# Kernel optimization log

Hardware: AMD Instinct MI355X
Metric: run time of the kernel (lower is better)

Reference implementation:

```python
import jax, jax.numpy as jnp
import numpy as np

B, T, D, H, DH, PD = 4, 1024, 1024, 16, 64, 4
DFF = 4 * D
EPS = 1e-5

# Plucker pair index vectors for point_dim=4: pairs (0,1),(0,2),(0,3),(1,2),(1,3),(2,3)
_PI = jnp.array([0, 0, 0, 1, 1, 2])
_PJ = jnp.array([1, 2, 3, 2, 3, 3])
_J6 = jnp.array([[0,0,0,0,0,1],[0,0,0,0,-1,0],[0,0,0,1,0,0],
                 [0,0,1,0,0,0],[0,-1,0,0,0,0],[1,0,0,0,0,0]], dtype=jnp.float32)

def layer_norm(x, g, b):
    mu = jnp.mean(x, axis=-1, keepdims=True)
    var = jnp.var(x, axis=-1, keepdims=True)
    return (x - mu) * jax.lax.rsqrt(var + EPS) * g + b

def exterior(p1, p2):
    # p1,p2: [B,T,H,4] -> normalized Plucker line [B,T,H,6]
    L = p1[..., _PI] * p2[..., _PJ] - p1[..., _PJ] * p2[..., _PI]
    n = jnp.maximum(jnp.linalg.norm(L, axis=-1, keepdims=True), 1e-12)
    return L / n

def linear(x, w, b=None):
    y = jnp.einsum('...i,oi->...o', x, w)
    return y + b if b is not None else y


def setup_inputs() -> dict:
    key = jax.random.key(0)
    ks = jax.random.split(key, 16)
    s = 0.02
    return {
        'x': jax.random.normal(ks[0], (B, T, D), jnp.float32),
        'ln1_g': jnp.ones((D,), jnp.float32), 'ln1_b': jnp.zeros((D,), jnp.float32),
        'qkv_w': jax.random.normal(ks[1], (3 * D, D), jnp.float32) * s,
        'qkv_b': jnp.zeros((3 * D,), jnp.float32),
        'w1w': jax.random.normal(ks[2], (PD * H, D), jnp.float32) * s,
        'w2w': jax.random.normal(ks[3], (PD * H, D), jnp.float32) * s,
        'w1r': jax.random.normal(ks[4], (PD * H, D), jnp.float32) * s,
        'w2r': jax.random.normal(ks[5], (PD * H, D), jnp.float32) * s,
        'memv_w': jax.random.normal(ks[6], (D, D), jnp.float32) * s,
        'memv_b': jnp.zeros((D,), jnp.float32),
        'memg_w': jax.random.normal(ks[7], (H, D), jnp.float32) * s,
        'memg_b': jnp.zeros((H,), jnp.float32),
        'mem_scale': jnp.full((H,), 0.1, jnp.float32),
        'out_w': jax.random.normal(ks[8], (D, D), jnp.float32) * s,
        'out_b': jnp.zeros((D,), jnp.float32),
        'decay_logits': jnp.full((H,), 4.6, jnp.float32),
        'ln2_g': jnp.ones((D,), jnp.float32), 'ln2_b': jnp.zeros((D,), jnp.float32),
        'fc1_w': jax.random.normal(ks[9], (DFF, D), jnp.float32) * s,
        'fc1_b': jnp.zeros((DFF,), jnp.float32),
        'fc2_w': jax.random.normal(ks[10], (D, DFF), jnp.float32) * s,
        'fc2_b': jnp.zeros((D,), jnp.float32),
    }


def attn_forward(h, qkv_w, qkv_b, w1w, w2w, w1r, w2r, memv_w, memv_b,
                 memg_w, memg_b, mem_scale, out_w, out_b, decay_logits):
    # Standard causal attention (dropout = identity, eval mode)
    qkv = linear(h, qkv_w, qkv_b).reshape(B, T, 3, H, DH)
    q, k, v = [jnp.transpose(qkv[:, :, i], (0, 2, 1, 3)) for i in range(3)]  # [B,H,T,dh]
    scores = jnp.einsum('bhqd,bhkd->bhqk', q, k) * (DH ** -0.5)
    causal_mask = jnp.triu(jnp.ones((T, T), bool), k=1)
    scores = jnp.where(causal_mask, -jnp.inf, scores)
    attn = jax.nn.softmax(scores, axis=-1)
    seq_out = jnp.einsum('bhqk,bhkd->bhqd', attn, v).transpose(0, 2, 1, 3).reshape(B, T, D)

    # Geometric incidence memory branch
    x_prev = jnp.concatenate([jnp.zeros((B, 1, D), h.dtype), h[:, :-1]], axis=1)
    w1 = linear(x_prev, w1w).reshape(B, T, H, PD)
    w2 = linear(h, w2w).reshape(B, T, H, PD)
    write_lines = exterior(w1, w2)                   # [B,T,H,6]
    r1 = linear(h, w1r).reshape(B, T, H, PD)
    r2 = linear(h, w2r).reshape(B, T, H, PD)
    read_lines = exterior(r1, r2)                    # [B,T,H,6]
    J_write = jnp.einsum('bthi,ij->bthj', write_lines, _J6)
    incidence = jnp.einsum('bihp,bjhp->bhij', read_lines, J_write)  # [B,H,T,T]
    inc_abs = jnp.abs(incidence)

    # per-head exponential decay over strictly-past positions (i > j)
    decays = jax.nn.sigmoid(decay_logits)            # [H]
    pos = jnp.arange(T, dtype=h.dtype)
    diffs = pos[:, None] - pos[None, :]              # [T,T]
    past = diffs > 0
    # decays**diffs, masked to strictly-past (subsumes the causal masked_fill on inc_abs)
    weights = jnp.where(past, decays[:, None, None] ** jnp.maximum(diffs, 0.0), 0.0)  # [H,T,T]
    mem_score = jnp.einsum('bhij,hij->bhi', inc_abs, weights)  # [B,H,T]

    mem_val = linear(h, memv_w, memv_b)              # [B,T,D]
    gate = jax.nn.sigmoid(linear(h, memg_w, memg_b)) # [B,T,H]
    gated = jax.nn.sigmoid(mem_score.transpose(0, 2, 1) * mem_scale) * gate
    gated = jnp.mean(gated, axis=-1, keepdims=True)  # [B,T,1]
    return linear(seq_out + gated * mem_val, out_w, out_b)


def reference(x, ln1_g, ln1_b, qkv_w, qkv_b, w1w, w2w, w1r, w2r,
              memv_w, memv_b, memg_w, memg_b, mem_scale, out_w, out_b,
              decay_logits, ln2_g, ln2_b, fc1_w, fc1_b, fc2_w, fc2_b):
    # Pre-LN transformer block: x + Attn(LN(x)); x + MLP(LN(x))
    h = layer_norm(x, ln1_g, ln1_b)
    x = x + attn_forward(h, qkv_w, qkv_b, w1w, w2w, w1r, w2r, memv_w, memv_b,
                         memg_w, memg_b, mem_scale, out_w, out_b, decay_logits)
    h2 = layer_norm(x, ln2_g, ln2_b)
    mlp = linear(jax.nn.gelu(linear(h2, fc1_w, fc1_b), approximate=False), fc2_w, fc2_b)
    return x + mlp
```

## Files before the change

kernel.cpp:

```cpp
#include <hip/hip_runtime.h>
#include <math.h>

typedef __bf16 bf16;
typedef float f32x4 __attribute__((ext_vector_type(4)));
typedef bf16 bf16x8 __attribute__((ext_vector_type(8)));
typedef bf16 bf16x4 __attribute__((ext_vector_type(4)));

#define DEV __device__ __forceinline__

DEV void async16(const void* g, void* s) {
  __builtin_amdgcn_global_load_lds(
      (const __attribute__((address_space(1))) unsigned int*)g,
      (__attribute__((address_space(3))) unsigned int*)s, 16, 0, 0);
}

DEV f32x4 mfma16(bf16x8 a, bf16x8 b, f32x4 c) {
  return __builtin_amdgcn_mfma_f32_16x16x32_bf16(a, b, c, 0, 0, 0);
}

DEV float sigf(float x) { return 1.0f / (1.0f + __expf(-x)); }

__global__ __launch_bounds__(256)
void cast_w_k(const float* __restrict__ qkv_w, const float* __restrict__ w1w,
              const float* __restrict__ w2w, const float* __restrict__ w1r,
              const float* __restrict__ w2r, const float* __restrict__ memg_w,
              const float* __restrict__ memv_w, const float* __restrict__ out_w,
              const float* __restrict__ fc1_w, const float* __restrict__ fc2_w,
              bf16* __restrict__ dst)
{
  const long i = ((long)blockIdx.x * 256 + threadIdx.x) * 4;
  if (i >= 14024704L) return;
  float4 v;
  if      (i < 3145728L)  v = *(const float4*)&qkv_w[i];
  else if (i < 3211264L)  v = *(const float4*)&w1w[i - 3145728L];
  else if (i < 3276800L)  v = *(const float4*)&w2w[i - 3211264L];
  else if (i < 3342336L)  v = *(const float4*)&w1r[i - 3276800L];
  else if (i < 3407872L)  v = *(const float4*)&w2r[i - 3342336L];
  else if (i < 3424256L)  v = *(const float4*)&memg_w[i - 3407872L];
  else if (i < 3538944L)  v = make_float4(0.f, 0.f, 0.f, 0.f);
  else if (i < 4587520L)  v = *(const float4*)&memv_w[i - 3538944L];
  else if (i < 5636096L)  v = *(const float4*)&out_w[i - 4587520L];
  else if (i < 9830400L)  v = *(const float4*)&fc1_w[i - 5636096L];
  else                    v = *(const float4*)&fc2_w[i - 9830400L];
  bf16x4 y;
  y[0] = (bf16)v.x; y[1] = (bf16)v.y; y[2] = (bf16)v.z; y[3] = (bf16)v.w;
  *(bf16x4*)&dst[i] = y;
}

__global__ __launch_bounds__(256)
void ln_k(const float* __restrict__ x, const float* __restrict__ g,
          const float* __restrict__ bb, bf16* __restrict__ out)
{
  const int row = blockIdx.x, tid = threadIdx.x;
  const float4 xv = ((const float4*)(x + (long)row * 1024))[tid];
  float s  = xv.x + xv.y + xv.z + xv.w;
  float ss = xv.x * xv.x + xv.y * xv.y + xv.z * xv.z + xv.w * xv.w;
#pragma unroll
  for (int off = 1; off < 64; off <<= 1) {
    s  += __shfl_xor(s, off);
    ss += __shfl_xor(ss, off);
  }
  __shared__ float red[8];
  const int wave = tid >> 6, lane = tid & 63;
  if (lane == 0) { red[wave] = s; red[4 + wave] = ss; }
  __syncthreads();
  s  = red[0] + red[1] + red[2] + red[3];
  ss = red[4] + red[5] + red[6] + red[7];
  const float mu  = s * (1.0f / 1024.0f);
  const float var = ss * (1.0f / 1024.0f) - mu * mu;
  const float inv = rsqrtf(var + 1e-5f);
  const float4 gv = ((const float4*)g)[tid];
  const float4 bv = ((const float4*)bb)[tid];
  bf16x4 y;
  y[0] = (bf16)((xv.x - mu) * inv * gv.x + bv.x);
  y[1] = (bf16)((xv.y - mu) * inv * gv.y + bv.y);
  y[2] = (bf16)((xv.z - mu) * inv * gv.z + bv.z);
  y[3] = (bf16)((xv.w - mu) * inv * gv.w + bv.w);
  *(bf16x4*)&out[(long)row * 1024 + tid * 4] = y;
}

enum { M_BIAS_RES = 0, M_GELU = 1 };

#define GEMM_CORE(Aptr, Bptr, Kloop, Kstride)                                \
  __shared__ __align__(16) bf16 As[128 * 32];                                \
  __shared__ __align__(16) bf16 Bs[128 * 32];                                \
  const int tid = threadIdx.x;                                               \
  const int wave = tid >> 6, lane = tid & 63;                                \
  const int fr = lane & 15, fq = lane >> 4;                                  \
  const long bm = (long)blockIdx.y * 128;                                    \
  const long bn = (long)blockIdx.x * 128;                                    \
  const int wm = (wave >> 1) * 64, wn = (wave & 1) * 64;                     \
  const int sr = wave * 16 + (lane >> 2);                                    \
  const int sc = (lane & 3) * 8;                                             \
  const bf16* ag0 = Aptr + (bm + sr) * (long)Kstride + sc;                   \
  const bf16* ag1 = Aptr + (bm + 64 + sr) * (long)Kstride + sc;              \
  const bf16* bg0 = Bptr + (bn + sr) * (long)Kstride + sc;                   \
  const bf16* bg1 = Bptr + (bn + 64 + sr) * (long)Kstride + sc;              \
  bf16* as0 = &As[(wave * 16) * 32];                                         \
  bf16* as1 = &As[(64 + wave * 16) * 32];                                    \
  bf16* bs0 = &Bs[(wave * 16) * 32];                                         \
  bf16* bs1 = &Bs[(64 + wave * 16) * 32];                                    \
  f32x4 acc[4][4] = {};                                                      \
  for (int kt = 0; kt < Kloop; kt += 32) {                                   \
    __syncthreads();                                                         \
    async16(ag0 + kt, as0);                                                  \
    async16(ag1 + kt, as1);                                                  \
    async16(bg0 + kt, bs0);                                                  \
    async16(bg1 + kt, bs1);                                                  \
    __syncthreads();                                                         \
    bf16x8 af[4], bfr[4];                                                    \
    _Pragma("unroll")                                                        \
    for (int i = 0; i < 4; ++i)                                              \
      af[i] = *(const bf16x8*)&As[(wm + i * 16 + fr) * 32 + fq * 8];         \
    _Pragma("unroll")                                                        \
    for (int j = 0; j < 4; ++j)                                              \
      bfr[j] = *(const bf16x8*)&Bs[(wn + j * 16 + fr) * 32 + fq * 8];        \
    _Pragma("unroll")                                                        \
    for (int i = 0; i < 4; ++i)                                              \
      _Pragma("unroll")                                                      \
      for (int j = 0; j < 4; ++j)                                            \
        acc[i][j] = mfma16(af[i], bfr[j], acc[i][j]);                        \
  }

template <int MODE>
__global__ __launch_bounds__(256, 2)
void gemm_k(const bf16* __restrict__ A, const bf16* __restrict__ Bw,
            int N, int K,
            const float* __restrict__ bias, const float* __restrict__ res,
            float* __restrict__ outf, bf16* __restrict__ outb)
{
  GEMM_CORE(A, Bw, K, K)
#pragma unroll
  for (int i = 0; i < 4; ++i) {
    const long row0 = bm + wm + i * 16 + fq * 4;
#pragma unroll
    for (int j = 0; j < 4; ++j) {
      const long col = bn + wn + j * 16 + fr;
#pragma unroll
      for (int r = 0; r < 4; ++r) {
        const long rr = row0 + r;
        float v = acc[i][j][r];
        if (MODE == M_BIAS_RES) {
          outf[rr * N + col] = v + bias[col] + res[rr * N + col];
        } else {
          v += bias[col];
          v = 0.5f * v * (1.0f + erff(v * 0.70710678118654752f));
          outb[rr * N + col] = (bf16)v;
        }
      }
    }
  }
}

__global__ __launch_bounds__(256, 2)
void gemm_fc2_k(const bf16* __restrict__ A_, const bf16* __restrict__ Bw_,
                float* __restrict__ part)
{
  const bf16* A  = A_  + (long)blockIdx.z * 2048;
  const bf16* Bw = Bw_ + (long)blockIdx.z * 2048;
  float* outf = part + (long)blockIdx.z * 4194304;
  GEMM_CORE(A, Bw, 2048, 4096)
#pragma unroll
  for (int i = 0; i < 4; ++i) {
    const long row0 = bm + wm + i * 16 + fq * 4;
#pragma unroll
    for (int j = 0; j < 4; ++j) {
      const long col = bn + wn + j * 16 + fr;
#pragma unroll
      for (int r = 0; r < 4; ++r)
        outf[(row0 + r) * 1024 + col] = acc[i][j][r];
    }
  }
}

__global__ __launch_bounds__(256)
void fc2red_k(const float* __restrict__ part, const float* __restrict__ x2,
              const float* __restrict__ fc2_b, float* __restrict__ out)
{
  const long row = blockIdx.x;
  const int tid = threadIdx.x;
  const long idx = row * 1024 + tid * 4;
  const float4 p0 = *(const float4*)&part[idx];
  const float4 p1 = *(const float4*)&part[idx + 4194304];
  const float4 xv = *(const float4*)&x2[idx];
  const float4 bv = *(const float4*)&fc2_b[tid * 4];
  float4 o;
  o.x = p0.x + p1.x + xv.x + bv.x;
  o.y = p0.y + p1.y + xv.y + bv.y;
  o.z = p0.z + p1.z + xv.z + bv.z;
  o.w = p0.w + p1.w + xv.w + bv.w;
  *(float4*)&out[idx] = o;
}

__global__ __launch_bounds__(256, 2)
void gemm3_k(const bf16* __restrict__ A, const bf16* __restrict__ Bw,
             const float* __restrict__ qkv_b, const float* __restrict__ memv_b,
             bf16* __restrict__ qk_out ,
             bf16* __restrict__ vt_out ,
             float* __restrict__ w4out ,
             float* __restrict__ memval )
{
  GEMM_CORE(A, Bw, 1024, 1024)
  if (bn < 3072) {
#pragma unroll
    for (int i = 0; i < 4; ++i) {
      const long row0 = bm + wm + i * 16 + fq * 4;
      const long b = row0 >> 10, t0 = row0 & 1023;
#pragma unroll
      for (int j = 0; j < 4; ++j) {
        const long col = bn + wn + j * 16 + fr;
        const long i3 = col >> 10;
        const long hh = (col >> 6) & 15;
        const long d  = col & 63;
        const float bs = qkv_b[col];
        if (i3 == 2) {
          bf16x4 y;
#pragma unroll
          for (int r = 0; r < 4; ++r) y[r] = (bf16)(acc[i][j][r] + bs);
          *(bf16x4*)&vt_out[((b * 16 + hh) * 64 + d) * 1024 + t0] = y;
        } else {
          const float sc2 = (i3 == 0) ? 0.125f : 1.0f;
          const long base = i3 * 4194304 + ((b * 16 + hh) * 1024 + t0) * 64 + d;
#pragma unroll
          for (int r = 0; r < 4; ++r)
            qk_out[base + r * 64] = (bf16)((acc[i][j][r] + bs) * sc2);
        }
      }
    }
  } else if (bn < 3456) {
#pragma unroll
    for (int i = 0; i < 4; ++i) {
      const long row0 = bm + wm + i * 16 + fq * 4;
#pragma unroll
      for (int j = 0; j < 4; ++j) {
        const long col = bn + wn + j * 16 + fr - 3072;
#pragma unroll
        for (int r = 0; r < 4; ++r)
          w4out[(row0 + r) * 384 + col] = acc[i][j][r];
      }
    }
  } else {
#pragma unroll
    for (int i = 0; i < 4; ++i) {
      const long row0 = bm + wm + i * 16 + fq * 4;
#pragma unroll
      for (int j = 0; j < 4; ++j) {
        const long col = bn + wn + j * 16 + fr - 3456;
        const float bs = memv_b[col];
#pragma unroll
        for (int r = 0; r < 4; ++r)
          memval[(row0 + r) * 1024 + col] = acc[i][j][r] + bs;
      }
    }
  }
}

__global__ __launch_bounds__(256, 3)
void attn_k(const bf16* __restrict__ q, const bf16* __restrict__ k,
            const bf16* __restrict__ vt, float* __restrict__ seq)
{
  __shared__ __align__(16) bf16 Ks[64 * 72];
  __shared__ __align__(16) bf16 Vs[64 * 72];
  __shared__ __align__(16) bf16 Ps[4][16 * 72];
  const int bx = blockIdx.x, h = blockIdx.y, b = blockIdx.z;
  const int tid = threadIdx.x;
  const int wave = tid >> 6, lane = tid & 63;
  const int fr = lane & 15, fq = lane >> 4;
  const long bh  = ((long)b * 16 + h) * 1024;
  const long bhv = ((long)b * 16 + h) * 64;

  for (int pass = 0; pass < 2; ++pass) {
    const int qt = pass ? 15 - bx : bx;
    const int qbase = qt * 64;
    const bf16x8 aq0 = *(const bf16x8*)&q[(bh + qbase + wave * 16 + fr) * 64 + fq * 8];
    const bf16x8 aq1 = *(const bf16x8*)&q[(bh + qbase + wave * 16 + fr) * 64 + 32 + fq * 8];

    f32x4 o[4] = {};
    float m_r[4] = {-1e30f, -1e30f, -1e30f, -1e30f};
    float l_r[4] = {0.0f, 0.0f, 0.0f, 0.0f};

    for (int kt = 0; kt <= qt; ++kt) {
      const int kb = kt * 64;
      __syncthreads();
#pragma unroll
      for (int rep = 0; rep < 2; ++rep) {
        const int c = rep * 256 + tid;
        const int key = c >> 3, seg = c & 7;
        *(bf16x8*)&Ks[key * 72 + seg * 8] =
            *(const bf16x8*)&k[(bh + kb + key) * 64 + seg * 8];
      }
#pragma unroll
      for (int rep = 0; rep < 2; ++rep) {
        const int c = rep * 256 + tid;
        const int d = c >> 3, seg = c & 7;
        *(bf16x8*)&Vs[d * 72 + seg * 8] =
            *(const bf16x8*)&vt[(bhv + d) * 1024 + kb + seg * 8];
      }
      __syncthreads();

      f32x4 s[4];
#pragma unroll
      for (int j = 0; j < 4; ++j) {
        const bf16x8 b0 = *(const bf16x8*)&Ks[(j * 16 + fr) * 72 + fq * 8];
        const bf16x8 b1 = *(const bf16x8*)&Ks[(j * 16 + fr) * 72 + 32 + fq * 8];
        f32x4 tacc = {};
        tacc = mfma16(aq0, b0, tacc);
        tacc = mfma16(aq1, b1, tacc);
        s[j] = tacc;
      }
      if (kt == qt) {
#pragma unroll
        for (int j = 0; j < 4; ++j)
#pragma unroll
          for (int r = 0; r < 4; ++r)
            if (kb + j * 16 + fr > qbase + wave * 16 + fq * 4 + r) s[j][r] = -1e30f;
      }

      float alpha[4];
#pragma unroll
      for (int r = 0; r < 4; ++r) {
        float t = fmaxf(fmaxf(s[0][r], s[1][r]), fmaxf(s[2][r], s[3][r]));
#pragma unroll
        for (int off = 1; off < 16; off <<= 1) t = fmaxf(t, __shfl_xor(t, off));
        const float mn = fmaxf(m_r[r], t);
        alpha[r] = __expf(m_r[r] - mn);
        m_r[r] = mn;
        float ls = 0.0f;
#pragma unroll
        for (int j = 0; j < 4; ++j) {
          const float p = __expf(s[j][r] - mn);
          s[j][r] = p;
          ls += p;
        }
#pragma unroll
        for (int off = 1; off < 16; off <<= 1) ls += __shfl_xor(ls, off);
        l_r[r] = l_r[r] * alpha[r] + ls;
#pragma unroll
        for (int jd = 0; jd < 4; ++jd) o[jd][r] *= alpha[r];
      }

#pragma unroll
      for (int j = 0; j < 4; ++j)
#pragma unroll
        for (int r = 0; r < 4; ++r)
          Ps[wave][(fq * 4 + r) * 72 + j * 16 + fr] = (bf16)s[j][r];

      const bf16x8 ap0 = *(const bf16x8*)&Ps[wave][fr * 72 + fq * 8];
      const bf16x8 ap1 = *(const bf16x8*)&Ps[wave][fr * 72 + 32 + fq * 8];
#pragma unroll
      for (int jd = 0; jd < 4; ++jd) {
        const bf16x8 b0 = *(const bf16x8*)&Vs[(jd * 16 + fr) * 72 + fq * 8];
        const bf16x8 b1 = *(const bf16x8*)&Vs[(jd * 16 + fr) * 72 + 32 + fq * 8];
        o[jd] = mfma16(ap0, b0, o[jd]);
        o[jd] = mfma16(ap1, b1, o[jd]);
      }
    }

#pragma unroll
    for (int r = 0; r < 4; ++r) {
      const long t_ = qbase + wave * 16 + fq * 4 + r;
      const float inv = 1.0f / l_r[r];
#pragma unroll
      for (int jd = 0; jd < 4; ++jd)
        seq[((long)b * 1024 + t_) * 1024 + h * 64 + jd * 16 + fr] = o[jd][r] * inv;
    }
  }
}

DEV void ext6(const float* p1, const float* p2, float* out) {
  const float L0 = p1[0] * p2[1] - p1[1] * p2[0];
  const float L1 = p1[0] * p2[2] - p1[2] * p2[0];
  const float L2 = p1[0] * p2[3] - p1[3] * p2[0];
  const float L3 = p1[1] * p2[2] - p1[2] * p2[1];
  const float L4 = p1[1] * p2[3] - p1[3] * p2[1];
  const float L5 = p1[2] * p2[3] - p1[3] * p2[2];
  const float nrm = sqrtf(L0*L0 + L1*L1 + L2*L2 + L3*L3 + L4*L4 + L5*L5);
  const float inv = 1.0f / fmaxf(nrm, 1e-12f);
  out[0] = L0 * inv; out[1] = L1 * inv; out[2] = L2 * inv;
  out[3] = L3 * inv; out[4] = L4 * inv; out[5] = L5 * inv;
}

__global__ __launch_bounds__(256)
void lines_k(const float* __restrict__ w4o, float* __restrict__ rl,
             float* __restrict__ jw)
{
  const int idx = blockIdx.x * 256 + threadIdx.x;
  const int hh = idx & 15;
  const int n  = idx >> 4;
  const int t  = n & 1023;
  const int b  = n >> 10;
  float p1[4], p2[4], wl[6], rv[6];
  if (t == 0) { p1[0] = p1[1] = p1[2] = p1[3] = 0.0f; }
  else {
    const float* s = w4o + (long)(n - 1) * 384 + hh * 4;
    p1[0] = s[0]; p1[1] = s[1]; p1[2] = s[2]; p1[3] = s[3];
  }
  { const float* s = w4o + (long)n * 384 + 64 + hh * 4;
    p2[0] = s[0]; p2[1] = s[1]; p2[2] = s[2]; p2[3] = s[3]; }
  ext6(p1, p2, wl);
  { const float* s = w4o + (long)n * 384 + 128 + hh * 4;
    p1[0] = s[0]; p1[1] = s[1]; p1[2] = s[2]; p1[3] = s[3]; }
  { const float* s = w4o + (long)n * 384 + 192 + hh * 4;
    p2[0] = s[0]; p2[1] = s[1]; p2[2] = s[2]; p2[3] = s[3]; }
  ext6(p1, p2, rv);
  const long dst = (((long)b * 16 + hh) * 1024 + t) * 6;
  jw[dst + 0] =  wl[5]; jw[dst + 1] = -wl[4]; jw[dst + 2] =  wl[3];
  jw[dst + 3] =  wl[2]; jw[dst + 4] = -wl[1]; jw[dst + 5] =  wl[0];
  rl[dst + 0] = rv[0]; rl[dst + 1] = rv[1]; rl[dst + 2] = rv[2];
  rl[dst + 3] = rv[3]; rl[dst + 4] = rv[4]; rl[dst + 5] = rv[5];
}

__global__ __launch_bounds__(256)
void memscore_k(const float* __restrict__ rl, const float* __restrict__ jw,
                const float* __restrict__ decay_logits, float* __restrict__ ms)
{
  __shared__ __align__(16) float jwS[256 * 8];
  const int IT[10] = {0,1,1,2,2,2,3,3,3,3};
  const int JC[10] = {0,0,1,0,1,2,0,1,2,3};
  const int it = IT[blockIdx.x], jc = JC[blockIdx.x];
  const int bh = blockIdx.y, hh = bh & 15;
  const float d = sigf(decay_logits[hh]);
  const float invd = 1.0f / d;
  const int j0 = jc * 256;
  const float* jwp = jw + (long)bh * 6144 + (long)j0 * 6;
#pragma unroll
  for (int rep = 0; rep < 8; ++rep) {
    const int c = rep * 256 + threadIdx.x;
    const int row = c >> 3, col = c & 7;
    jwS[c] = (col < 6) ? jwp[row * 6 + col] : 0.0f;
  }
  __syncthreads();
  const int i = it * 256 + threadIdx.x;
  const float* rlp = rl + (long)bh * 6144 + (long)i * 6;
  const float r0 = rlp[0], r1 = rlp[1], r2 = rlp[2];
  const float r3 = rlp[3], r4 = rlp[4], r5 = rlp[5];
  const int nj = (jc == it) ? (int)threadIdx.x : 256;
  float w = __expf(__logf(d) * (float)(i - j0));
  float s = 0.0f;
  for (int jj = 0; jj < nj; ++jj) {
    const float* row = &jwS[jj * 8];
    const float dot = r0 * row[0] + r1 * row[1] + r2 * row[2] +
                      r3 * row[3] + r4 * row[4] + r5 * row[5];
    s += fabsf(dot) * w;
    w *= invd;
  }
  atomicAdd(&ms[(long)bh * 1024 + i], s);
}

__global__ __launch_bounds__(256)
void combine_k(const float* __restrict__ seq, const float* __restrict__ memval,
               const float* __restrict__ w4o, const float* __restrict__ ms,
               const float* __restrict__ memg_b, const float* __restrict__ mem_scale,
               bf16* __restrict__ comb)
{
  const int n = blockIdx.x;
  const int b = n >> 10, t = n & 1023;
  const int tid = threadIdx.x;
  __shared__ float gsh;
  if (tid < 16) {
    const int hh = tid;
    const float gate = sigf(w4o[(long)n * 384 + 256 + hh] + memg_b[hh]);
    float val = sigf(ms[((long)(b * 16 + hh)) * 1024 + t] * mem_scale[hh]) * gate;
#pragma unroll
    for (int off = 1; off < 16; off <<= 1) val += __shfl_xor(val, off);
    if (tid == 0) gsh = val * (1.0f / 16.0f);
  }
  __syncthreads();
  const float g = gsh;
  const float4 sv = ((const float4*)(seq + (long)n * 1024))[tid];
  const float4 mv = ((const float4*)(memval + (long)n * 1024))[tid];
  bf16x4 y;
  y[0] = (bf16)(sv.x + g * mv.x);
  y[1] = (bf16)(sv.y + g * mv.y);
  y[2] = (bf16)(sv.z + g * mv.z);
  y[3] = (bf16)(sv.w + g * mv.w);
  *(bf16x4*)&comb[(long)n * 1024 + tid * 4] = y;
}

extern "C" void kernel_launch(void* const* d_in, const int* in_sizes, int n_in,
                              void* d_out, int out_size, void* d_ws, size_t ws_size,
                              hipStream_t stream) {
  (void)in_sizes; (void)n_in; (void)out_size; (void)ws_size;
  const float* x         = (const float*)d_in[0];
  const float* ln1_g     = (const float*)d_in[1];
  const float* ln1_b     = (const float*)d_in[2];
  const float* qkv_w     = (const float*)d_in[3];
  const float* qkv_b     = (const float*)d_in[4];
  const float* w1w       = (const float*)d_in[5];
  const float* w2w       = (const float*)d_in[6];
  const float* w1r       = (const float*)d_in[7];
  const float* w2r       = (const float*)d_in[8];
  const float* memv_w    = (const float*)d_in[9];
  const float* memv_b    = (const float*)d_in[10];
  const float* memg_w    = (const float*)d_in[11];
  const float* memg_b    = (const float*)d_in[12];
  const float* mem_scale = (const float*)d_in[13];
  const float* out_w     = (const float*)d_in[14];
  const float* out_b     = (const float*)d_in[15];
  const float* decay_l   = (const float*)d_in[16];
  const float* ln2_g     = (const float*)d_in[17];
  const float* ln2_b     = (const float*)d_in[18];
  const float* fc1_w     = (const float*)d_in[19];
  const float* fc1_b     = (const float*)d_in[20];
  const float* fc2_w     = (const float*)d_in[21];
  const float* fc2_b     = (const float*)d_in[22];

  char* ws = (char*)d_ws;
  bf16*  Wbf    = (bf16*)ws;
  bf16*  Wout   = Wbf + 4587520;
  bf16*  Wfc1   = Wbf + 5636096;
  bf16*  Wfc2   = Wbf + 9830400;
  bf16*  h_bf   = (bf16*)(ws + 28049408);
  bf16*  q_bf   = (bf16*)(ws + 36438016);
  bf16*  vt_bf  = q_bf + 2 * 4194304;
  float* seq    = (float*)(ws + 61603840);
  bf16*  fc1out = q_bf;
  float* w4out  = (float*)(ws + 78381056);
  float* rl     = (float*)(ws + 84672512);
  float* jwb    = (float*)(ws + 86245376);
  float* msb    = (float*)(ws + 87818240);
  float* memval = (float*)(ws + 88080384);
  bf16*  comb   = (bf16*)(ws + 104857600);
  float* x2     = (float*)(ws + 113246208);
  float* fc2part = (float*)(ws + 78381056);

  cast_w_k<<<13696, 256, 0, stream>>>(qkv_w, w1w, w2w, w1r, w2r, memg_w,
                                      memv_w, out_w, fc1_w, fc2_w, Wbf);
  ln_k<<<4096, 256, 0, stream>>>(x, ln1_g, ln1_b, h_bf);
  gemm3_k<<<dim3(35, 32), 256, 0, stream>>>(h_bf, Wbf, qkv_b, memv_b,
                                            q_bf, vt_bf, w4out, memval);
  attn_k<<<dim3(8, 16, 4), 256, 0, stream>>>(q_bf, q_bf + 4194304, vt_bf, seq);
  lines_k<<<256, 256, 0, stream>>>(w4out, rl, jwb);
  hipMemsetAsync(msb, 0, 64 * 1024 * sizeof(float), stream);
  memscore_k<<<dim3(10, 64), 256, 0, stream>>>(rl, jwb, decay_l, msb);
  combine_k<<<4096, 256, 0, stream>>>(seq, memval, w4out, msb, memg_b,
                                      mem_scale, comb);
  gemm_k<M_BIAS_RES><<<dim3(8, 32), 256, 0, stream>>>(comb, Wout, 1024, 1024,
                                                      out_b, x, x2, nullptr);
  ln_k<<<4096, 256, 0, stream>>>(x2, ln2_g, ln2_b, h_bf);
  gemm_k<M_GELU><<<dim3(32, 32), 256, 0, stream>>>(h_bf, Wfc1, 4096, 1024,
                                                   fc1_b, nullptr, nullptr, fc1out);
  gemm_fc2_k<<<dim3(8, 32, 2), 256, 0, stream>>>(fc1out, Wfc2, fc2part);
  fc2red_k<<<4096, 256, 0, stream>>>(fc2part, x2, fc2_b, (float*)d_out);
}
```

Baseline: 440.0 us.

## Fuse memory gating into attention epilogue, split-K out-proj with fused LN2

After: 433.3 us. About the same (-1.5%).

```diff
diff --git a/kernel.cpp b/kernel.cpp
--- a/kernel.cpp
+++ b/kernel.cpp
@@ -77,6 +77,50 @@
   y[2] = (bf16)((xv.z - mu) * inv * gv.z + bv.z);
   y[3] = (bf16)((xv.w - mu) * inv * gv.w + bv.w);
   *(bf16x4*)&out[(long)row * 1024 + tid * 4] = y;
+}
+
+__global__ __launch_bounds__(256)
+void ln2red_k(const float* __restrict__ part, const float* __restrict__ out_b,
+              const float* __restrict__ x, const float* __restrict__ g,
+              const float* __restrict__ bb, float* __restrict__ x2,
+              bf16* __restrict__ h)
+{
+  const int row = blockIdx.x, tid = threadIdx.x;
+  const long idx = (long)row * 1024 + tid * 4;
+  const float4 p0 = *(const float4*)&part[idx];
+  const float4 p1 = *(const float4*)&part[idx + 4194304];
+  const float4 xr = *(const float4*)&x[idx];
+  const float4 ob = *(const float4*)&out_b[tid * 4];
+  float4 xv;
+  xv.x = p0.x + p1.x + xr.x + ob.x;
+  xv.y = p0.y + p1.y + xr.y + ob.y;
+  xv.z = p0.z + p1.z + xr.z + ob.z;
+  xv.w = p0.w + p1.w + xr.w + ob.w;
+  *(float4*)&x2[idx] = xv;
+  float s  = xv.x + xv.y + xv.z + xv.w;
+  float ss = xv.x * xv.x + xv.y * xv.y + xv.z * xv.z + xv.w * xv.w;
+#pragma unroll
+  for (int off = 1; off < 64; off <<= 1) {
+    s  += __shfl_xor(s, off);
+    ss += __shfl_xor(ss, off);
+  }
+  __shared__ float red[8];
+  const int wave = tid >> 6, lane = tid & 63;
+  if (lane == 0) { red[wave] = s; red[4 + wave] = ss; }
+  __syncthreads();
+  s  = red[0] + red[1] + red[2] + red[3];
+  ss = red[4] + red[5] + red[6] + red[7];
+  const float mu  = s * (1.0f / 1024.0f);
+  const float var = ss * (1.0f / 1024.0f) - mu * mu;
+  const float inv = rsqrtf(var + 1e-5f);
+  const float4 gv = ((const float4*)g)[tid];
+  const float4 bv = ((const float4*)bb)[tid];
+  bf16x4 y;
+  y[0] = (bf16)((xv.x - mu) * inv * gv.x + bv.x);
+  y[1] = (bf16)((xv.y - mu) * inv * gv.y + bv.y);
+  y[2] = (bf16)((xv.z - mu) * inv * gv.z + bv.z);
+  y[3] = (bf16)((xv.w - mu) * inv * gv.w + bv.w);
+  *(bf16x4*)&h[idx] = y;
 }
 
 enum { M_BIAS_RES = 0, M_GELU = 1 };
@@ -123,7 +167,7 @@
   }
 
 template <int MODE>
-__global__ __launch_bounds__(256, 2)
+__global__ __launch_bounds__(256, 4)
 void gemm_k(const bf16* __restrict__ A, const bf16* __restrict__ Bw,
             int N, int K,
             const float* __restrict__ bias, const float* __restrict__ res,
@@ -152,14 +196,15 @@
   }
 }
 
-__global__ __launch_bounds__(256, 2)
-void gemm_fc2_k(const bf16* __restrict__ A_, const bf16* __restrict__ Bw_,
-                float* __restrict__ part)
-{
-  const bf16* A  = A_  + (long)blockIdx.z * 2048;
-  const bf16* Bw = Bw_ + (long)blockIdx.z * 2048;
+template <int KLEN, int KSTRIDE>
+__global__ __launch_bounds__(256, 4)
+void gemm_splitk_k(const bf16* __restrict__ A_, const bf16* __restrict__ Bw_,
+                   float* __restrict__ part)
+{
+  const bf16* A  = A_  + (long)blockIdx.z * KLEN;
+  const bf16* Bw = Bw_ + (long)blockIdx.z * KLEN;
   float* outf = part + (long)blockIdx.z * 4194304;
-  GEMM_CORE(A, Bw, 2048, 4096)
+  GEMM_CORE(A, Bw, KLEN, KSTRIDE)
 #pragma unroll
   for (int i = 0; i < 4; ++i) {
     const long row0 = bm + wm + i * 16 + fq * 4;
@@ -192,7 +237,7 @@
   *(float4*)&out[idx] = o;
 }
 
-__global__ __launch_bounds__(256, 2)
+__global__ __launch_bounds__(256, 4)
 void gemm3_k(const bf16* __restrict__ A, const bf16* __restrict__ Bw,
              const float* __restrict__ qkv_b, const float* __restrict__ memv_b,
              bf16* __restrict__ qk_out ,
@@ -257,7 +302,8 @@
 
 __global__ __launch_bounds__(256, 3)
 void attn_k(const bf16* __restrict__ q, const bf16* __restrict__ k,
-            const bf16* __restrict__ vt, float* __restrict__ seq)
+            const bf16* __restrict__ vt, const float* __restrict__ memval,
+            const float* __restrict__ gbuf, bf16* __restrict__ comb)
 {
   __shared__ __align__(16) bf16 Ks[64 * 72];
   __shared__ __align__(16) bf16 Vs[64 * 72];
@@ -359,10 +405,15 @@
 #pragma unroll
     for (int r = 0; r < 4; ++r) {
       const long t_ = qbase + wave * 16 + fq * 4 + r;
+      const long row = (long)b * 1024 + t_;
       const float inv = 1.0f / l_r[r];
-#pragma unroll
-      for (int jd = 0; jd < 4; ++jd)
-        seq[((long)b * 1024 + t_) * 1024 + h * 64 + jd * 16 + fr] = o[jd][r] * inv;
+      const float gv = gbuf[row];
+#pragma unroll
+      for (int jd = 0; jd < 4; ++jd) {
+        const long col = h * 64 + jd * 16 + fr;
+        comb[row * 1024 + col] =
+            (bf16)(o[jd][r] * inv + gv * memval[row * 1024 + col]);
+      }
     }
   }
 }
@@ -381,66 +432,50 @@
 }
 
 __global__ __launch_bounds__(256)
-void lines_k(const float* __restrict__ w4o, float* __restrict__ rl,
-             float* __restrict__ jw)
-{
-  const int idx = blockIdx.x * 256 + threadIdx.x;
-  const int hh = idx & 15;
-  const int n  = idx >> 4;
-  const int t  = n & 1023;
-  const int b  = n >> 10;
-  float p1[4], p2[4], wl[6], rv[6];
-  if (t == 0) { p1[0] = p1[1] = p1[2] = p1[3] = 0.0f; }
-  else {
-    const float* s = w4o + (long)(n - 1) * 384 + hh * 4;
-    p1[0] = s[0]; p1[1] = s[1]; p1[2] = s[2]; p1[3] = s[3];
-  }
-  { const float* s = w4o + (long)n * 384 + 64 + hh * 4;
-    p2[0] = s[0]; p2[1] = s[1]; p2[2] = s[2]; p2[3] = s[3]; }
-  ext6(p1, p2, wl);
-  { const float* s = w4o + (long)n * 384 + 128 + hh * 4;
-    p1[0] = s[0]; p1[1] = s[1]; p1[2] = s[2]; p1[3] = s[3]; }
-  { const float* s = w4o + (long)n * 384 + 192 + hh * 4;
-    p2[0] = s[0]; p2[1] = s[1]; p2[2] = s[2]; p2[3] = s[3]; }
-  ext6(p1, p2, rv);
-  const long dst = (((long)b * 16 + hh) * 1024 + t) * 6;
-  jw[dst + 0] =  wl[5]; jw[dst + 1] = -wl[4]; jw[dst + 2] =  wl[3];
-  jw[dst + 3] =  wl[2]; jw[dst + 4] = -wl[1]; jw[dst + 5] =  wl[0];
-  rl[dst + 0] = rv[0]; rl[dst + 1] = rv[1]; rl[dst + 2] = rv[2];
-  rl[dst + 3] = rv[3]; rl[dst + 4] = rv[4]; rl[dst + 5] = rv[5];
-}
-
-__global__ __launch_bounds__(256)
-void memscore_k(const float* __restrict__ rl, const float* __restrict__ jw,
+void memscore_k(const float* __restrict__ w4o,
                 const float* __restrict__ decay_logits, float* __restrict__ ms)
 {
   __shared__ __align__(16) float jwS[256 * 8];
   const int IT[10] = {0,1,1,2,2,2,3,3,3,3};
   const int JC[10] = {0,0,1,0,1,2,0,1,2,3};
   const int it = IT[blockIdx.x], jc = JC[blockIdx.x];
-  const int bh = blockIdx.y, hh = bh & 15;
+  const int bh = blockIdx.y, hh = bh & 15, b = bh >> 4;
   const float d = sigf(decay_logits[hh]);
   const float invd = 1.0f / d;
   const int j0 = jc * 256;
-  const float* jwp = jw + (long)bh * 6144 + (long)j0 * 6;
-#pragma unroll
-  for (int rep = 0; rep < 8; ++rep) {
-    const int c = rep * 256 + threadIdx.x;
-    const int row = c >> 3, col = c & 7;
-    jwS[c] = (col < 6) ? jwp[row * 6 + col] : 0.0f;
+  {
+    const int j = j0 + threadIdx.x;
+    const long nj = (long)b * 1024 + j;
+    float p1[4], p2[4], wl[6];
+    if (j == 0) { p1[0] = p1[1] = p1[2] = p1[3] = 0.0f; }
+    else {
+      const float* s = w4o + (nj - 1) * 384 + hh * 4;
+      p1[0] = s[0]; p1[1] = s[1]; p1[2] = s[2]; p1[3] = s[3];
+    }
+    { const float* s = w4o + nj * 384 + 64 + hh * 4;
+      p2[0] = s[0]; p2[1] = s[1]; p2[2] = s[2]; p2[3] = s[3]; }
+    ext6(p1, p2, wl);
+    float* dstS = &jwS[threadIdx.x * 8];
+    dstS[0] =  wl[5]; dstS[1] = -wl[4]; dstS[2] =  wl[3];
+    dstS[3] =  wl[2]; dstS[4] = -wl[1]; dstS[5] =  wl[0];
+    dstS[6] = 0.0f;   dstS[7] = 0.0f;
   }
   __syncthreads();
   const int i = it * 256 + threadIdx.x;
-  const float* rlp = rl + (long)bh * 6144 + (long)i * 6;
-  const float r0 = rlp[0], r1 = rlp[1], r2 = rlp[2];
-  const float r3 = rlp[3], r4 = rlp[4], r5 = rlp[5];
+  const long ni = (long)b * 1024 + i;
+  float q1[4], q2[4], rv[6];
+  { const float* s = w4o + ni * 384 + 128 + hh * 4;
+    q1[0] = s[0]; q1[1] = s[1]; q1[2] = s[2]; q1[3] = s[3]; }
+  { const float* s = w4o + ni * 384 + 192 + hh * 4;
+    q2[0] = s[0]; q2[1] = s[1]; q2[2] = s[2]; q2[3] = s[3]; }
+  ext6(q1, q2, rv);
   const int nj = (jc == it) ? (int)threadIdx.x : 256;
   float w = __expf(__logf(d) * (float)(i - j0));
   float s = 0.0f;
   for (int jj = 0; jj < nj; ++jj) {
     const float* row = &jwS[jj * 8];
-    const float dot = r0 * row[0] + r1 * row[1] + r2 * row[2] +
-                      r3 * row[3] + r4 * row[4] + r5 * row[5];
+    const float dot = rv[0] * row[0] + rv[1] * row[1] + rv[2] * row[2] +
+                      rv[3] * row[3] + rv[4] * row[4] + rv[5] * row[5];
     s += fabsf(dot) * w;
     w *= invd;
   }
@@ -448,33 +483,19 @@
 }
 
 __global__ __launch_bounds__(256)
-void combine_k(const float* __restrict__ seq, const float* __restrict__ memval,
-               const float* __restrict__ w4o, const float* __restrict__ ms,
-               const float* __restrict__ memg_b, const float* __restrict__ mem_scale,
-               bf16* __restrict__ comb)
-{
-  const int n = blockIdx.x;
+void gate_k(const float* __restrict__ w4o, const float* __restrict__ ms,
+            const float* __restrict__ memg_b, const float* __restrict__ mem_scale,
+            float* __restrict__ g)
+{
+  const int n = blockIdx.x * 256 + threadIdx.x;
   const int b = n >> 10, t = n & 1023;
-  const int tid = threadIdx.x;
-  __shared__ float gsh;
-  if (tid < 16) {
-    const int hh = tid;
-    const float gate = sigf(w4o[(long)n * 384 + 256 + hh] + memg_b[hh]);
-    float val = sigf(ms[((long)(b * 16 + hh)) * 1024 + t] * mem_scale[hh]) * gate;
-#pragma unroll
-    for (int off = 1; off < 16; off <<= 1) val += __shfl_xor(val, off);
-    if (tid == 0) gsh = val * (1.0f / 16.0f);
-  }
-  __syncthreads();
-  const float g = gsh;
-  const float4 sv = ((const float4*)(seq + (long)n * 1024))[tid];
-  const float4 mv = ((const float4*)(memval + (long)n * 1024))[tid];
-  bf16x4 y;
-  y[0] = (bf16)(sv.x + g * mv.x);
-  y[1] = (bf16)(sv.y + g * mv.y);
-  y[2] = (bf16)(sv.z + g * mv.z);
-  y[3] = (bf16)(sv.w + g * mv.w);
-  *(bf16x4*)&comb[(long)n * 1024 + tid * 4] = y;
+  float acc = 0.0f;
+#pragma unroll
+  for (int h = 0; h < 16; ++h) {
+    const float gate = sigf(w4o[(long)n * 384 + 256 + h] + memg_b[h]);
+    acc += sigf(ms[((long)(b * 16 + h)) * 1024 + t] * mem_scale[h]) * gate;
+  }
+  g[n] = acc * (1.0f / 16.0f);
 }
 
 extern "C" void kernel_launch(void* const* d_in, const int* in_sizes, int n_in,
@@ -513,33 +534,32 @@
   bf16*  h_bf   = (bf16*)(ws + 28049408);
   bf16*  q_bf   = (bf16*)(ws + 36438016);
   bf16*  vt_bf  = q_bf + 2 * 4194304;
-  float* seq    = (float*)(ws + 61603840);
+  float* oppart = (float*)(ws + 36438016);
   bf16*  fc1out = q_bf;
   float* w4out  = (float*)(ws + 78381056);
-  float* rl     = (float*)(ws + 84672512);
-  float* jwb    = (float*)(ws + 86245376);
-  float* msb    = (float*)(ws + 87818240);
+  float* msb    = (float*)(ws + 84672512);
+  float* gbuf   = (float*)(ws + 84934656);
   float* memval = (float*)(ws + 88080384);
+  float* fc2part = (float*)(ws + 69992448);
   bf16*  comb   = (bf16*)(ws + 104857600);
   float* x2     = (float*)(ws + 113246208);
-  float* fc2part = (float*)(ws + 78381056);
 
   cast_w_k<<<13696, 256, 0, stream>>>(qkv_w, w1w, w2w, w1r, w2r, memg_w,
                                       memv_w, out_w, fc1_w, fc2_w, Wbf);
   ln_k<<<4096, 256, 0, stream>>>(x, ln1_g, ln1_b, h_bf);
   gemm3_k<<<dim3(35, 32), 256, 0, stream>>>(h_bf, Wbf, qkv_b, memv_b,
                                             q_bf, vt_bf, w4out, memval);
-  attn_k<<<dim3(8, 16, 4), 256, 0, stream>>>(q_bf, q_bf + 4194304, vt_bf, seq);
-  lines_k<<<256, 256, 0, stream>>>(w4out, rl, jwb);
   hipMemsetAsync(msb, 0, 64 * 1024 * sizeof(float), stream);
-  memscore_k<<<dim3(10, 64), 256, 0, stream>>>(rl, jwb, decay_l, msb);
-  combine_k<<<4096, 256, 0, stream>>>(seq, memval, w4out, msb, memg_b,
-                                      mem_scale, comb);
-  gemm_k<M_BIAS_RES><<<dim3(8, 32), 256, 0, stream>>>(comb, Wout, 1024, 1024,
-                                                      out_b, x, x2, nullptr);
-  ln_k<<<4096, 256, 0, stream>>>(x2, ln2_g, ln2_b, h_bf);
+  memscore_k<<<dim3(10, 64), 256, 0, stream>>>(w4out, decay_l, msb);
+  gate_k<<<16, 256, 0, stream>>>(w4out, msb, memg_b, mem_scale, gbuf);
+  attn_k<<<dim3(8, 16, 4), 256, 0, stream>>>(q_bf, q_bf + 4194304, vt_bf,
+                                             memval, gbuf, comb);
+  gemm_splitk_k<512, 1024><<<dim3(8, 32, 2), 256, 0, stream>>>(comb, Wout,
+                                                               oppart);
+  ln2red_k<<<4096, 256, 0, stream>>>(oppart, out_b, x, ln2_g, ln2_b, x2, h_bf);
   gemm_k<M_GELU><<<dim3(32, 32), 256, 0, stream>>>(h_bf, Wfc1, 4096, 1024,
                                                    fc1_b, nullptr, nullptr, fc1out);
-  gemm_fc2_k<<<dim3(8, 32, 2), 256, 0, stream>>>(fc1out, Wfc2, fc2part);
+  gemm_splitk_k<2048, 4096><<<dim3(8, 32, 2), 256, 0, stream>>>(fc1out, Wfc2,
+                                                                fc2part);
   fc2red_k<<<4096, 256, 0, stream>>>(fc2part, x2, fc2_b, (float*)d_out);
 }
```
